# Kernel optimization log

Measured on AMD Instinct MI355X. Metric: run time of the kernel, lower is better.

## Reference

```python
import jax, jax.numpy as jnp
import numpy as np

WEIGHT_GRADIENT = 0.05
EPS = 1e-6


def _normalize(q, eps):
    # torch F.normalize: q / max(||q||, eps)
    n = jnp.sqrt(jnp.sum(q * q, axis=1, keepdims=True))
    return q / jnp.maximum(n, eps)


def _grad_mag(q, eps):
    # depthwise conv with [-1,1] kernels == finite differences, then replicate-pad
    gx = q[..., :, 1:] - q[..., :, :-1]          # (B,4,H,W-1)
    gy = q[..., 1:, :] - q[..., :-1, :]          # (B,4,H-1,W)
    gx = jnp.pad(gx, ((0, 0), (0, 0), (0, 0), (0, 1)), mode='edge')
    gy = jnp.pad(gy, ((0, 0), (0, 0), (0, 1), (0, 0)), mode='edge')
    return jnp.sqrt(gx * gx + gy * gy + eps)


def setup_inputs() -> dict:
    key = jax.random.key(0)
    k1, k2, k3 = jax.random.split(key, 3)
    B, H, W, S = 16, 256, 256, 24
    q_pred = jax.random.normal(k1, (B, 4, H, W), dtype=jnp.float32)
    q_target = jax.random.normal(k2, (B, 4, H, W), dtype=jnp.float32)
    syms = jax.random.normal(k3, (S, 4), dtype=jnp.float32)
    syms = syms / jnp.linalg.norm(syms, axis=1, keepdims=True)  # unit quaternions
    return {"q_pred": q_pred, "q_target": q_target, "syms": syms}


def reference(q_pred, q_target, syms, eps=EPS):
    # (B,4,H,W) -> (N,4)
    qp = _normalize(q_pred.transpose(0, 2, 3, 1).reshape(-1, 4), eps)
    qt = _normalize(q_target.transpose(0, 2, 3, 1).reshape(-1, 4), eps)
    w1, x1, y1, z1 = qp[:, 0], qp[:, 1], qp[:, 2], qp[:, 3]
    w2, x2, y2, z2 = qt[:, 0], qt[:, 1], qt[:, 2], qt[:, 3]
    # relative quaternion r = qt * conj(qp)
    rw = w2 * w1 + x2 * x1 + y2 * y1 + z2 * z1
    rx = -w2 * x1 + x2 * w1 - y2 * z1 + z2 * y1
    ry = -w2 * y1 + x2 * z1 + y2 * w1 - z2 * x1
    rz = -w2 * z1 - x2 * y1 + y2 * x1 + z2 * w1
    r4 = jnp.stack([rw, rx, ry, rz], axis=1)                 # (N,4)
    signs = jnp.array([1.0, -1.0, -1.0, -1.0], dtype=syms.dtype)
    # w_dist[n,s] = rw*s_w - rx*s_x - ry*s_y - rz*s_z
    w_dist = jnp.einsum('nc,sc->ns', r4, syms * signs)       # (N,S)
    max_w = jnp.max(jnp.abs(w_dist), axis=1)
    max_w = jnp.clip(max_w, -(1.0 - eps), 1.0 - eps)
    loss_rot = jnp.mean(2.0 * jnp.arccos(max_w))
    gp = _grad_mag(q_pred, eps)
    gt = _grad_mag(q_target, eps)
    loss_grad = jnp.mean(jnp.abs(gp - gt))
    return loss_rot + WEIGHT_GRADIENT * loss_grad
```

## Files before the change

kernel.cpp:

```cpp
#include <hip/hip_runtime.h>
#include <math.h>

constexpr int Hc = 256;
constexpr int Wc = 256;
constexpr float EPSf = 1e-6f;

__device__ __forceinline__ float comp(const float4& v, int p) {
    return p == 0 ? v.x : p == 1 ? v.y : p == 2 ? v.z : v.w;
}

__device__ __forceinline__ float fast_acos01(float x) {
    float t = __builtin_amdgcn_sqrtf(1.0f - x);
    float p = fmaf(fmaf(fmaf(-0.0187293f, x, 0.0742610f), x, -0.2121144f),
                   x, 1.5707288f);
    return t * p;
}

__device__ __forceinline__ float fast_sqrt(float x) {
    return __builtin_amdgcn_sqrtf(x);
}

template<int S>
__global__ __launch_bounds__(256, 4) void sym_loss_main(
    const float* __restrict__ qp,
    const float* __restrict__ qt,
    const float* __restrict__ syms,
    float2* __restrict__ partial)
{
    __shared__ float lds[2 * 4 * 4 * 256];

    int tid  = threadIdx.x;
    int lane = tid & 63;
    int wid  = tid >> 6;
    int row  = (blockIdx.x << 2) + wid;
    int b    = row >> 8;
    int h    = row & (Hc - 1);
    int w0   = lane << 2;

    int idx0 = (b << 18) + (h << 8) + w0;
    int dy   = (h == Hc - 1) ? -Wc : Wc;
    int xw   = w0 + ((lane == 63) ? 2 : 4);

    float4 Cp[4], Ct[4], Yp3[4], Yt3[4];
    #pragma unroll
    for (int c = 0; c < 4; ++c) {
        int idx = idx0 + (c << 16);
        Cp[c] = *(const float4*)(qp + idx);
        Ct[c] = *(const float4*)(qt + idx);
    }
    if (wid == 3) {
        #pragma unroll
        for (int c = 0; c < 4; ++c) {
            int idx = idx0 + (c << 16) + dy;
            Yp3[c] = *(const float4*)(qp + idx);
            Yt3[c] = *(const float4*)(qt + idx);
        }
    }

    #pragma unroll
    for (int c = 0; c < 4; ++c) {
        *(float4*)&lds[(((0 * 4 + c) * 4 + wid) << 8) + w0] = Cp[c];
        *(float4*)&lds[(((1 * 4 + c) * 4 + wid) << 8) + w0] = Ct[c];
    }
    __syncthreads();

    float gsum = 0.0f;
    #pragma unroll
    for (int c = 0; c < 4; ++c) {
        float4 C = Cp[c], D = Ct[c];
        float4 Y, Z;
        if (wid < 3) {
            Y = *(const float4*)&lds[(((0 * 4 + c) * 4 + wid + 1) << 8) + w0];
            Z = *(const float4*)&lds[(((1 * 4 + c) * 4 + wid + 1) << 8) + w0];
        } else {
            Y = Yp3[c]; Z = Yt3[c];
        }
        float xp = lds[(((0 * 4 + c) * 4 + wid) << 8) + xw];
        float xt = lds[(((1 * 4 + c) * 4 + wid) << 8) + xw];

        float gx, gy, a, e;
        gx = C.y - C.x; gy = Y.x - C.x;
        a = fast_sqrt(fmaf(gx, gx, fmaf(gy, gy, EPSf)));
        gx = D.y - D.x; gy = Z.x - D.x;
        e = fast_sqrt(fmaf(gx, gx, fmaf(gy, gy, EPSf)));
        gsum += fabsf(a - e);

        gx = C.z - C.y; gy = Y.y - C.y;
        a = fast_sqrt(fmaf(gx, gx, fmaf(gy, gy, EPSf)));
        gx = D.z - D.y; gy = Z.y - D.y;
        e = fast_sqrt(fmaf(gx, gx, fmaf(gy, gy, EPSf)));
        gsum += fabsf(a - e);

        gx = C.w - C.z; gy = Y.z - C.z;
        a = fast_sqrt(fmaf(gx, gx, fmaf(gy, gy, EPSf)));
        gx = D.w - D.z; gy = Z.z - D.z;
        e = fast_sqrt(fmaf(gx, gx, fmaf(gy, gy, EPSf)));
        gsum += fabsf(a - e);

        gx = xp - C.w;  gy = Y.w - C.w;
        a = fast_sqrt(fmaf(gx, gx, fmaf(gy, gy, EPSf)));
        gx = xt - D.w;  gy = Z.w - D.w;
        e = fast_sqrt(fmaf(gx, gx, fmaf(gy, gy, EPSf)));
        gsum += fabsf(a - e);
    }

    float rw[4], nx[4], ny[4], nz[4];
    #pragma unroll
    for (int p = 0; p < 4; ++p) {
        float a0 = comp(Cp[0], p), a1 = comp(Cp[1], p),
              a2 = comp(Cp[2], p), a3 = comp(Cp[3], p);
        float b0 = comp(Ct[0], p), b1 = comp(Ct[1], p),
              b2 = comp(Ct[2], p), b3 = comp(Ct[3], p);

        float ss1 = fmaf(a0, a0, fmaf(a1, a1, fmaf(a2, a2, a3 * a3)));
        float ss2 = fmaf(b0, b0, fmaf(b1, b1, fmaf(b2, b2, b3 * b3)));
        float i1 = __builtin_amdgcn_rsqf(ss1);
        float i2 = __builtin_amdgcn_rsqf(ss2);
        float w1 = a0 * i1, x1 = a1 * i1, y1 = a2 * i1, z1 = a3 * i1;
        float w2 = b0 * i2, x2 = b1 * i2, y2 = b2 * i2, z2 = b3 * i2;

        rw[p] =  w2 * w1 + x2 * x1 + y2 * y1 + z2 * z1;
        float rx = -w2 * x1 + x2 * w1 - y2 * z1 + z2 * y1;
        float ry = -w2 * y1 + x2 * z1 + y2 * w1 - z2 * x1;
        float rz = -w2 * z1 - x2 * y1 + y2 * x1 + z2 * w1;
        nx[p] = -rx; ny[p] = -ry; nz[p] = -rz;
    }

    const float4* __restrict__ sv4 = (const float4*)syms;
    float maxw[4] = {0.f, 0.f, 0.f, 0.f};
    #pragma unroll
    for (int s = 0; s < S; ++s) {
        float4 sv = sv4[s];
        #pragma unroll
        for (int p = 0; p < 4; ++p) {
            float d = fmaf(nz[p], sv.w,
                      fmaf(ny[p], sv.z,
                      fmaf(nx[p], sv.y, rw[p] * sv.x)));
            maxw[p] = fmaxf(maxw[p], fabsf(d));
        }
    }
    float rot = 0.0f;
    #pragma unroll
    for (int p = 0; p < 4; ++p)
        rot += fast_acos01(fminf(maxw[p], 1.0f - EPSf));

    #pragma unroll
    for (int off = 32; off > 0; off >>= 1) {
        rot  += __shfl_down(rot,  off, 64);
        gsum += __shfl_down(gsum, off, 64);
    }
    __shared__ float s_r[4], s_g[4];
    if (lane == 0) { s_r[wid] = rot; s_g[wid] = gsum; }
    __syncthreads();
    if (tid == 0) {
        float2 o;
        o.x = s_r[0] + s_r[1] + s_r[2] + s_r[3];
        o.y = s_g[0] + s_g[1] + s_g[2] + s_g[3];
        partial[blockIdx.x] = o;
    }
}

__global__ __launch_bounds__(256) void sym_loss_generic(
    const float* __restrict__ qp,
    const float* __restrict__ qt,
    const float* __restrict__ syms,
    int S,
    float2* __restrict__ partial)
{
    int t    = blockIdx.x * 256 + threadIdx.x;
    int lane = t & 63;
    int row  = t >> 6;
    int b    = row >> 8;
    int h    = row & (Hc - 1);
    int w0   = lane << 2;
    int idx0 = (b << 18) + (h << 8) + w0;
    int dy = (h == Hc - 1) ? -Wc : Wc;
    int xo = (lane == 63) ? 2 : 4;

    float4 Cp[4], Yp[4], Ct[4], Yt[4];
    float  xp[4], xt[4];
    #pragma unroll
    for (int c = 0; c < 4; ++c) {
        int idx = idx0 + (c << 16);
        Cp[c] = *(const float4*)(qp + idx);
        Yp[c] = *(const float4*)(qp + idx + dy);
        xp[c] = qp[idx + xo];
        Ct[c] = *(const float4*)(qt + idx);
        Yt[c] = *(const float4*)(qt + idx + dy);
        xt[c] = qt[idx + xo];
    }
    float gsum = 0.0f;
    #pragma unroll
    for (int c = 0; c < 4; ++c) {
        float4 C = Cp[c], Y = Yp[c], D = Ct[c], Z = Yt[c];
        float gx, gy, a, e;
        gx = C.y - C.x; gy = Y.x - C.x;
        a = fast_sqrt(fmaf(gx, gx, fmaf(gy, gy, EPSf)));
        gx = D.y - D.x; gy = Z.x - D.x;
        e = fast_sqrt(fmaf(gx, gx, fmaf(gy, gy, EPSf)));
        gsum += fabsf(a - e);
        gx = C.z - C.y; gy = Y.y - C.y;
        a = fast_sqrt(fmaf(gx, gx, fmaf(gy, gy, EPSf)));
        gx = D.z - D.y; gy = Z.y - D.y;
        e = fast_sqrt(fmaf(gx, gx, fmaf(gy, gy, EPSf)));
        gsum += fabsf(a - e);
        gx = C.w - C.z; gy = Y.z - C.z;
        a = fast_sqrt(fmaf(gx, gx, fmaf(gy, gy, EPSf)));
        gx = D.w - D.z; gy = Z.z - D.z;
        e = fast_sqrt(fmaf(gx, gx, fmaf(gy, gy, EPSf)));
        gsum += fabsf(a - e);
        gx = xp[c] - C.w; gy = Y.w - C.w;
        a = fast_sqrt(fmaf(gx, gx, fmaf(gy, gy, EPSf)));
        gx = xt[c] - D.w; gy = Z.w - D.w;
        e = fast_sqrt(fmaf(gx, gx, fmaf(gy, gy, EPSf)));
        gsum += fabsf(a - e);
    }
    float rw[4], nx[4], ny[4], nz[4];
    #pragma unroll
    for (int p = 0; p < 4; ++p) {
        float a0 = comp(Cp[0], p), a1 = comp(Cp[1], p),
              a2 = comp(Cp[2], p), a3 = comp(Cp[3], p);
        float b0 = comp(Ct[0], p), b1 = comp(Ct[1], p),
              b2 = comp(Ct[2], p), b3 = comp(Ct[3], p);
        float ss1 = fmaf(a0, a0, fmaf(a1, a1, fmaf(a2, a2, a3 * a3)));
        float ss2 = fmaf(b0, b0, fmaf(b1, b1, fmaf(b2, b2, b3 * b3)));
        float i1 = __builtin_amdgcn_rsqf(ss1);
        float i2 = __builtin_amdgcn_rsqf(ss2);
        float w1 = a0 * i1, x1 = a1 * i1, y1 = a2 * i1, z1 = a3 * i1;
        float w2 = b0 * i2, x2 = b1 * i2, y2 = b2 * i2, z2 = b3 * i2;
        rw[p] =  w2 * w1 + x2 * x1 + y2 * y1 + z2 * z1;
        float rx = -w2 * x1 + x2 * w1 - y2 * z1 + z2 * y1;
        float ry = -w2 * y1 + x2 * z1 + y2 * w1 - z2 * x1;
        float rz = -w2 * z1 - x2 * y1 + y2 * x1 + z2 * w1;
        nx[p] = -rx; ny[p] = -ry; nz[p] = -rz;
    }
    const float4* __restrict__ sv4 = (const float4*)syms;
    float maxw[4] = {0.f, 0.f, 0.f, 0.f};
    for (int s = 0; s < S; ++s) {
        float4 sv = sv4[s];
        #pragma unroll
        for (int p = 0; p < 4; ++p) {
            float d = fmaf(nz[p], sv.w,
                      fmaf(ny[p], sv.z,
                      fmaf(nx[p], sv.y, rw[p] * sv.x)));
            maxw[p] = fmaxf(maxw[p], fabsf(d));
        }
    }
    float rot = 0.0f;
    #pragma unroll
    for (int p = 0; p < 4; ++p)
        rot += fast_acos01(fminf(maxw[p], 1.0f - EPSf));
    #pragma unroll
    for (int off = 32; off > 0; off >>= 1) {
        rot  += __shfl_down(rot,  off, 64);
        gsum += __shfl_down(gsum, off, 64);
    }
    __shared__ float s_r[4], s_g[4];
    int wid = threadIdx.x >> 6;
    if ((threadIdx.x & 63) == 0) { s_r[wid] = rot; s_g[wid] = gsum; }
    __syncthreads();
    if (threadIdx.x == 0) {
        float2 o;
        o.x = s_r[0] + s_r[1] + s_r[2] + s_r[3];
        o.y = s_g[0] + s_g[1] + s_g[2] + s_g[3];
        partial[blockIdx.x] = o;
    }
}

__global__ __launch_bounds__(256) void sym_loss_reduce(
    const float2* __restrict__ partial, int nblocks,
    float* __restrict__ out, double cRot, double cGrad)
{
    double r = 0.0, g = 0.0;
    for (int i = threadIdx.x; i < nblocks; i += 256) {
        float2 p = partial[i];
        r += (double)p.x;
        g += (double)p.y;
    }
    #pragma unroll
    for (int off = 32; off > 0; off >>= 1) {
        r += __shfl_down(r, off, 64);
        g += __shfl_down(g, off, 64);
    }
    __shared__ double s_r[4], s_g[4];
    int wid = threadIdx.x >> 6;
    if ((threadIdx.x & 63) == 0) { s_r[wid] = r; s_g[wid] = g; }
    __syncthreads();
    if (threadIdx.x == 0) {
        double rr = s_r[0] + s_r[1] + s_r[2] + s_r[3];
        double gg = s_g[0] + s_g[1] + s_g[2] + s_g[3];
        out[0] = (float)(rr * cRot + gg * cGrad);
    }
}

extern "C" void kernel_launch(void* const* d_in, const int* in_sizes, int n_in,
                              void* d_out, int out_size, void* d_ws, size_t ws_size,
                              hipStream_t stream)
{
    const float* qp   = (const float*)d_in[0];
    const float* qt   = (const float*)d_in[1];
    const float* syms = (const float*)d_in[2];

    int S  = in_sizes[2] / 4;
    int NP = in_sizes[0] / 4;

    float2* partial = (float2*)d_ws;

    double cRot  = 2.0 / (double)NP;
    double cGrad = 0.05 / ((double)NP * 4.0);

    int nblocks;
    if (S == 24) {
        nblocks = NP / 1024;
        sym_loss_main<24><<<nblocks, 256, 0, stream>>>(qp, qt, syms, partial);
    } else {
        nblocks = (NP / 4) / 256;
        sym_loss_generic<<<nblocks, 256, 0, stream>>>(qp, qt, syms, S, partial);
    }

    sym_loss_reduce<<<1, 256, 0, stream>>>(partial, nblocks, (float*)d_out,
                                           cRot, cGrad);
}
```

Before: 88.85 us.

## Fuse final reduction into main kernel and drop LDS neighbor exchange

The main kernel now reduces the block partials itself: each block bumps an atomic counter, and the last block to finish sums all partials in double and writes the output. This removes the separate reduce kernel launch but adds a hipMemsetAsync to reset the counter. The LDS staging and __syncthreads used to share neighbour rows are replaced by direct global loads of the row below and the right-edge element, which relies on cache hits for the duplicated reads. The change also remaps block IDs with an XCD-style interleave and restructures the symmetry loop into float2 pairs, possibly to encourage packed math.

```diff
diff --git a/kernel.cpp b/kernel.cpp
--- a/kernel.cpp
+++ b/kernel.cpp
@@ -25,59 +25,42 @@
     const float* __restrict__ qp,
     const float* __restrict__ qt,
     const float* __restrict__ syms,
-    float2* __restrict__ partial)
+    float2* __restrict__ partial,
+    unsigned int* __restrict__ cnt,
+    float* __restrict__ out,
+    double cRot, double cGrad)
 {
-    __shared__ float lds[2 * 4 * 4 * 256];
-
-    int tid  = threadIdx.x;
-    int lane = tid & 63;
-    int wid  = tid >> 6;
-    int row  = (blockIdx.x << 2) + wid;
+    int nb  = gridDim.x;
+    int lid = (blockIdx.x & 7) * (nb >> 3) + (blockIdx.x >> 3);
+
+    int t    = lid * 256 + threadIdx.x;
+    int lane = t & 63;
+    int row  = t >> 6;
     int b    = row >> 8;
     int h    = row & (Hc - 1);
     int w0   = lane << 2;
 
     int idx0 = (b << 18) + (h << 8) + w0;
-    int dy   = (h == Hc - 1) ? -Wc : Wc;
-    int xw   = w0 + ((lane == 63) ? 2 : 4);
-
-    float4 Cp[4], Ct[4], Yp3[4], Yt3[4];
+    int dy = (h == Hc - 1) ? -Wc : Wc;
+    int xo = (lane == 63) ? 2 : 4;
+
+    float4 Cp[4], Yp[4], Ct[4], Yt[4];
+    float  xp[4], xt[4];
     #pragma unroll
     for (int c = 0; c < 4; ++c) {
         int idx = idx0 + (c << 16);
         Cp[c] = *(const float4*)(qp + idx);
+        Yp[c] = *(const float4*)(qp + idx + dy);
+        xp[c] = qp[idx + xo];
         Ct[c] = *(const float4*)(qt + idx);
-    }
-    if (wid == 3) {
-        #pragma unroll
-        for (int c = 0; c < 4; ++c) {
-            int idx = idx0 + (c << 16) + dy;
-            Yp3[c] = *(const float4*)(qp + idx);
-            Yt3[c] = *(const float4*)(qt + idx);
-        }
-    }
-
+        Yt[c] = *(const float4*)(qt + idx + dy);
+        xt[c] = qt[idx + xo];
+    }
+
+    float gsum = 0.0f;
     #pragma unroll
     for (int c = 0; c < 4; ++c) {
-        *(float4*)&lds[(((0 * 4 + c) * 4 + wid) << 8) + w0] = Cp[c];
-        *(float4*)&lds[(((1 * 4 + c) * 4 + wid) << 8) + w0] = Ct[c];
-    }
-    __syncthreads();
-
-    float gsum = 0.0f;
-    #pragma unroll
-    for (int c = 0; c < 4; ++c) {
-        float4 C = Cp[c], D = Ct[c];
-        float4 Y, Z;
-        if (wid < 3) {
-            Y = *(const float4*)&lds[(((0 * 4 + c) * 4 + wid + 1) << 8) + w0];
-            Z = *(const float4*)&lds[(((1 * 4 + c) * 4 + wid + 1) << 8) + w0];
-        } else {
-            Y = Yp3[c]; Z = Yt3[c];
-        }
-        float xp = lds[(((0 * 4 + c) * 4 + wid) << 8) + xw];
-        float xt = lds[(((1 * 4 + c) * 4 + wid) << 8) + xw];
-
+        float4 C = Cp[c], Y = Yp[c], D = Ct[c], Z = Yt[c];
         float gx, gy, a, e;
         gx = C.y - C.x; gy = Y.x - C.x;
         a = fast_sqrt(fmaf(gx, gx, fmaf(gy, gy, EPSf)));
@@ -97,9 +80,9 @@
         e = fast_sqrt(fmaf(gx, gx, fmaf(gy, gy, EPSf)));
         gsum += fabsf(a - e);
 
-        gx = xp - C.w;  gy = Y.w - C.w;
-        a = fast_sqrt(fmaf(gx, gx, fmaf(gy, gy, EPSf)));
-        gx = xt - D.w;  gy = Z.w - D.w;
+        gx = xp[c] - C.w; gy = Y.w - C.w;
+        a = fast_sqrt(fmaf(gx, gx, fmaf(gy, gy, EPSf)));
+        gx = xt[c] - D.w; gy = Z.w - D.w;
         e = fast_sqrt(fmaf(gx, gx, fmaf(gy, gy, EPSf)));
         gsum += fabsf(a - e);
     }
@@ -127,22 +110,28 @@
     }
 
     const float4* __restrict__ sv4 = (const float4*)syms;
-    float maxw[4] = {0.f, 0.f, 0.f, 0.f};
+    float2 rwA = {rw[0], rw[1]}, rwB = {rw[2], rw[3]};
+    float2 nxA = {nx[0], nx[1]}, nxB = {nx[2], nx[3]};
+    float2 nyA = {ny[0], ny[1]}, nyB = {ny[2], ny[3]};
+    float2 nzA = {nz[0], nz[1]}, nzB = {nz[2], nz[3]};
+    float2 mA = {0.f, 0.f}, mB = {0.f, 0.f};
     #pragma unroll
     for (int s = 0; s < S; ++s) {
         float4 sv = sv4[s];
-        #pragma unroll
-        for (int p = 0; p < 4; ++p) {
-            float d = fmaf(nz[p], sv.w,
-                      fmaf(ny[p], sv.z,
-                      fmaf(nx[p], sv.y, rw[p] * sv.x)));
-            maxw[p] = fmaxf(maxw[p], fabsf(d));
-        }
-    }
-    float rot = 0.0f;
-    #pragma unroll
-    for (int p = 0; p < 4; ++p)
-        rot += fast_acos01(fminf(maxw[p], 1.0f - EPSf));
+        float2 dA, dB;
+        dA.x = fmaf(nzA.x, sv.w, fmaf(nyA.x, sv.z, fmaf(nxA.x, sv.y, rwA.x * sv.x)));
+        dA.y = fmaf(nzA.y, sv.w, fmaf(nyA.y, sv.z, fmaf(nxA.y, sv.y, rwA.y * sv.x)));
+        dB.x = fmaf(nzB.x, sv.w, fmaf(nyB.x, sv.z, fmaf(nxB.x, sv.y, rwB.x * sv.x)));
+        dB.y = fmaf(nzB.y, sv.w, fmaf(nyB.y, sv.z, fmaf(nxB.y, sv.y, rwB.y * sv.x)));
+        mA.x = fmaxf(mA.x, fabsf(dA.x));
+        mA.y = fmaxf(mA.y, fabsf(dA.y));
+        mB.x = fmaxf(mB.x, fabsf(dB.x));
+        mB.y = fmaxf(mB.y, fabsf(dB.y));
+    }
+    float rot = fast_acos01(fminf(mA.x, 1.0f - EPSf))
+              + fast_acos01(fminf(mA.y, 1.0f - EPSf))
+              + fast_acos01(fminf(mB.x, 1.0f - EPSf))
+              + fast_acos01(fminf(mB.y, 1.0f - EPSf));
 
     #pragma unroll
     for (int off = 32; off > 0; off >>= 1) {
@@ -150,13 +139,41 @@
         gsum += __shfl_down(gsum, off, 64);
     }
     __shared__ float s_r[4], s_g[4];
-    if (lane == 0) { s_r[wid] = rot; s_g[wid] = gsum; }
+    __shared__ bool amLast;
+    int wid = threadIdx.x >> 6;
+    if ((threadIdx.x & 63) == 0) { s_r[wid] = rot; s_g[wid] = gsum; }
     __syncthreads();
-    if (tid == 0) {
+    if (threadIdx.x == 0) {
         float2 o;
         o.x = s_r[0] + s_r[1] + s_r[2] + s_r[3];
         o.y = s_g[0] + s_g[1] + s_g[2] + s_g[3];
-        partial[blockIdx.x] = o;
+        partial[lid] = o;
+        __threadfence();
+        unsigned int old = atomicAdd(cnt, 1u);
+        amLast = (old == (unsigned int)(nb - 1));
+    }
+    __syncthreads();
+    if (amLast) {
+        __threadfence();
+        double r = 0.0, g = 0.0;
+        for (int i = threadIdx.x; i < nb; i += 256) {
+            float2 p = partial[i];
+            r += (double)p.x;
+            g += (double)p.y;
+        }
+        #pragma unroll
+        for (int off = 32; off > 0; off >>= 1) {
+            r += __shfl_down(r, off, 64);
+            g += __shfl_down(g, off, 64);
+        }
+        __shared__ double d_r[4], d_g[4];
+        if ((threadIdx.x & 63) == 0) { d_r[wid] = r; d_g[wid] = g; }
+        __syncthreads();
+        if (threadIdx.x == 0) {
+            double rr = d_r[0] + d_r[1] + d_r[2] + d_r[3];
+            double gg = d_g[0] + d_g[1] + d_g[2] + d_g[3];
+            out[0] = (float)(rr * cRot + gg * cGrad);
+        }
     }
 }
 
@@ -303,21 +320,22 @@
 
     int S  = in_sizes[2] / 4;
     int NP = in_sizes[0] / 4;
+    int nblocks = (NP / 4) / 256;
 
     float2* partial = (float2*)d_ws;
+    unsigned int* cnt = (unsigned int*)((char*)d_ws + nblocks * sizeof(float2));
 
     double cRot  = 2.0 / (double)NP;
     double cGrad = 0.05 / ((double)NP * 4.0);
 
-    int nblocks;
+    hipMemsetAsync(cnt, 0, sizeof(unsigned int), stream);
+
     if (S == 24) {
-        nblocks = NP / 1024;
-        sym_loss_main<24><<<nblocks, 256, 0, stream>>>(qp, qt, syms, partial);
+        sym_loss_main<24><<<nblocks, 256, 0, stream>>>(
+            qp, qt, syms, partial, cnt, (float*)d_out, cRot, cGrad);
     } else {
-        nblocks = (NP / 4) / 256;
         sym_loss_generic<<<nblocks, 256, 0, stream>>>(qp, qt, syms, S, partial);
-    }
-
-    sym_loss_reduce<<<1, 256, 0, stream>>>(partial, nblocks, (float*)d_out,
-                                           cRot, cGrad);
-}
+        sym_loss_reduce<<<1, 256, 0, stream>>>(partial, nblocks, (float*)d_out,
+                                               cRot, cGrad);
+    }
+}
```

Result: slower. 105.5 us (+18.8%).
